# Performance work log

Hardware: AMD Instinct MI355X
Metric: run time of the kernel (lower is better)

Reference implementation:

```python
import jax, jax.numpy as jnp
import numpy as np

N_NODES = 50000
N_EDGES = 800000
NUM_GRAPHS = 512
IN_DIM = 128
HID = 128
OUT_DIM = 1


def setup_inputs() -> dict:
    key = jax.random.key(0)
    ks = jax.random.split(key, 8)
    x = jax.random.normal(ks[0], (N_NODES, IN_DIM), dtype=jnp.float32)
    edge_index = jax.random.randint(ks[1], (2, N_EDGES), 0, N_NODES, dtype=jnp.int64)
    batch = jnp.sort(jax.random.randint(ks[2], (N_NODES,), 0, NUM_GRAPHS, dtype=jnp.int64))
    s1 = 1.0 / np.sqrt(IN_DIM)
    s2 = 1.0 / np.sqrt(HID)
    W1 = jax.random.normal(ks[3], (IN_DIM, HID), dtype=jnp.float32) * s1
    b1 = jnp.zeros((HID,), dtype=jnp.float32)
    W2 = jax.random.normal(ks[4], (HID, HID), dtype=jnp.float32) * s2
    b2 = jnp.zeros((HID,), dtype=jnp.float32)
    Wl = jax.random.normal(ks[5], (HID, OUT_DIM), dtype=jnp.float32) * s2
    bl = jnp.zeros((OUT_DIM,), dtype=jnp.float32)
    return {"x": x, "edge_index": edge_index, "batch": batch,
            "W1": W1, "b1": b1, "W2": W2, "b2": b2, "Wl": Wl, "bl": bl}


def _gcn_conv(x, src, dst, norm, W, b):
    # GCNConv: D^{-1/2}(A+I)D^{-1/2} X W + b (self-loops already in src/dst)
    h = x @ W                                    # [N, H]
    msg = h[src] * norm[:, None]                 # gather + edge-normalize
    agg = jax.ops.segment_sum(msg, dst, num_segments=N_NODES)  # scatter-add
    return agg + b


def reference(x, edge_index, batch, W1, b1, W2, b2, Wl, bl):
    loops = jnp.arange(N_NODES, dtype=edge_index.dtype)
    src = jnp.concatenate([edge_index[0], loops])
    dst = jnp.concatenate([edge_index[1], loops])
    deg = jax.ops.segment_sum(jnp.ones_like(dst, dtype=x.dtype), dst, num_segments=N_NODES)
    dinv = jax.lax.rsqrt(deg)                    # deg >= 1 due to self-loops
    norm = dinv[src] * dinv[dst]                 # symmetric normalization per edge

    h = jax.nn.relu(_gcn_conv(x, src, dst, norm, W1, b1))
    h = jax.nn.relu(_gcn_conv(h, src, dst, norm, W2, b2))

    # global_mean_pool over graph ids
    sums = jax.ops.segment_sum(h, batch, num_segments=NUM_GRAPHS)
    cnts = jax.ops.segment_sum(jnp.ones((N_NODES,), dtype=h.dtype), batch, num_segments=NUM_GRAPHS)
    pooled = sums / jnp.maximum(cnts, 1.0)[:, None]

    out = jax.nn.sigmoid(pooled @ Wl + bl)       # [G, 1]
    return out.squeeze(1)                        # [G]
```

## Files before the change

### kernel.cpp

```cpp
#include <hip/hip_runtime.h>
#include <hip/hip_bf16.h>

#define N_NODES 50000
#define N_EDGES 800000
#define NUM_GRAPHS 512
#define MAXDEG 64
#define EPB 4096
#define P1_BLOCKS 196
#define NBUCK 256
#define NPB 196

typedef short short8 __attribute__((ext_vector_type(8)));
typedef unsigned short u16x8 __attribute__((ext_vector_type(8)));
typedef float f32x4 __attribute__((ext_vector_type(4)));

__device__ __forceinline__ unsigned short f2bu(float f) {
    __hip_bfloat16 h = __float2bfloat16(f);
    return *reinterpret_cast<unsigned short*>(&h);
}
__device__ __forceinline__ float bu2f(unsigned short u) {
    unsigned int v = ((unsigned int)u) << 16;
    float f;
    __builtin_memcpy(&f, &v, 4);
    return f;
}

__global__ __launch_bounds__(256) void bin_k(const int* __restrict__ ei,
                                             unsigned int* __restrict__ staging,
                                             int* __restrict__ cnts_tbl,
                                             int* __restrict__ offs_tbl,
                                             unsigned short* __restrict__ hs1,
                                             unsigned short* __restrict__ hs2) {
    __shared__ unsigned int st[EPB];
    __shared__ int cnt[NBUCK], cur[NBUCK], scan[NBUCK];
    int b = blockIdx.x, t = threadIdx.x;
    if (b == 0 && t < 64)
        ((unsigned int*)(hs1 + (size_t)N_NODES * 128))[t] = 0u;
    if (b == 1 && t < 64)
        ((unsigned int*)(hs2 + (size_t)N_NODES * 128))[t] = 0u;
    cnt[t] = 0;
    __syncthreads();

    int e0 = b * EPB;
    int srcv[16], dstv[16], bk[16];
#pragma unroll
    for (int k = 0; k < 16; ++k) {
        int e = e0 + k * 256 + t;
        bool ok = e < N_EDGES;
        srcv[k] = ok ? ei[e] : 0;
        dstv[k] = ok ? ei[N_EDGES + e] : 0;
        bk[k] = ok ? (dstv[k] / NPB) : -1;
        if (ok) atomicAdd(&cnt[bk[k]], 1);
    }
    __syncthreads();
    scan[t] = cnt[t];
    __syncthreads();
    for (int off = 1; off < 256; off <<= 1) {
        int u = t >= off ? scan[t - off] : 0;
        __syncthreads();
        scan[t] += u;
        __syncthreads();
    }
    int excl = scan[t] - cnt[t];
    cur[t] = excl;
    cnts_tbl[t * P1_BLOCKS + b] = cnt[t];
    offs_tbl[t * P1_BLOCKS + b] = excl;
    __syncthreads();
#pragma unroll
    for (int k = 0; k < 16; ++k) {
        if (bk[k] >= 0) {
            int pos = atomicAdd(&cur[bk[k]], 1);
            int dl = dstv[k] - bk[k] * NPB;
            st[pos] = (unsigned int)srcv[k] | ((unsigned int)dl << 16);
        }
    }
    __syncthreads();
    unsigned int* gout = staging + (size_t)b * EPB;
    for (int i = t; i < EPB; i += 256) gout[i] = st[i];
}

__global__ __launch_bounds__(256) void adjbuild_k(const unsigned int* __restrict__ staging,
                                                  const int* __restrict__ cnts_tbl,
                                                  const int* __restrict__ offs_tbl,
                                                  unsigned short* __restrict__ adj,
                                                  int* __restrict__ cnt,
                                                  float* __restrict__ dinv,
                                                  const float* __restrict__ W1,
                                                  const float* __restrict__ W2,
                                                  unsigned short* __restrict__ W1t,
                                                  unsigned short* __restrict__ W2t) {
    int b = blockIdx.x, t = threadIdx.x;
    if (b >= NBUCK) {
        int wb = b - NBUCK;
        const float* W = wb < 64 ? W1 : W2;
        unsigned short* Wt = wb < 64 ? W1t : W2t;
        int idx = (wb & 63) * 256 + t;
        int k = idx >> 7, n = idx & 127;
        Wt[n * 128 + k] = f2bu(W[idx]);
        return;
    }
    __shared__ unsigned short adjL[NPB * MAXDEG];
    __shared__ int cntL[NPB];
    __shared__ int segStart[P1_BLOCKS + 1];
    __shared__ int segOff[P1_BLOCKS];
    __shared__ int tmp[256];

    if (t < NPB) cntL[t] = 0;
    int c = t < P1_BLOCKS ? cnts_tbl[b * P1_BLOCKS + t] : 0;
    if (t < P1_BLOCKS) segOff[t] = offs_tbl[b * P1_BLOCKS + t];
    tmp[t] = c;
    __syncthreads();
    for (int off = 1; off < 256; off <<= 1) {
        int u = t >= off ? tmp[t - off] : 0;
        __syncthreads();
        tmp[t] += u;
        __syncthreads();
    }
    if (t < P1_BLOCKS) segStart[t] = tmp[t] - c;
    if (t == 0) segStart[P1_BLOCKS] = tmp[P1_BLOCKS - 1];
    __syncthreads();

    int T = segStart[P1_BLOCKS];
    for (int f = t; f < T; f += 256) {
        int lo = 0, hi = P1_BLOCKS;
        while (hi - lo > 1) {
            int m = (lo + hi) >> 1;
            if (segStart[m] <= f) lo = m; else hi = m;
        }
        unsigned int p = staging[(size_t)lo * EPB + segOff[lo] + (f - segStart[lo])];
        int src = p & 0xFFFF;
        int dl = p >> 16;
        int slot = atomicAdd(&cntL[dl], 1);
        if (slot < MAXDEG - 1) adjL[dl * MAXDEG + slot] = (unsigned short)src;
    }
    __syncthreads();

    int nodeBase = b * NPB;
    if (t < NPB) {
        int node = nodeBase + t;
        int cc = cntL[t];
        int ec = cc < MAXDEG - 1 ? cc : MAXDEG - 1;
        adjL[t * MAXDEG + ec] = (unsigned short)node;
        int tot = ec + 1, tot4 = (tot + 3) & ~3;
        for (int s = tot; s < tot4; ++s) adjL[t * MAXDEG + s] = (unsigned short)N_NODES;
        if (node < N_NODES) {
            cnt[node] = cc;
            dinv[node] = rsqrtf((float)cc + 1.0f);
        }
    }
    __syncthreads();
    unsigned int* g = (unsigned int*)(adj + (size_t)nodeBase * MAXDEG);
    const unsigned int* l = (const unsigned int*)adjL;
    for (int i = t; i < NPB * MAXDEG / 2; i += 256) g[i] = l[i];
}

__global__ __launch_bounds__(256) void gemm_k(const float* __restrict__ Ap,
                                              const unsigned short* __restrict__ Wt,
                                              const float* __restrict__ dinv,
                                              unsigned short* __restrict__ C) {
    __shared__ unsigned short Wl[128 * 136];
    int t = threadIdx.x;
    for (int idx = t; idx < 2048; idx += 256) {
        int n = idx >> 4, c = idx & 15;
        *(u16x8*)(Wl + n * 136 + c * 8) = *(const u16x8*)(Wt + n * 128 + c * 8);
    }
    __syncthreads();

    int wave = t >> 6, lane = t & 63, quad = lane >> 4, ln = lane & 15;
    int rb = blockIdx.x * 128 + wave * 16;

    short8 a[2][4];
#pragma unroll
    for (int mt = 0; mt < 2; ++mt) {
        int r = rb + mt * 64 + ln;
        r = r < N_NODES ? r : N_NODES - 1;
        const float* arow = Ap + (size_t)r * 128 + quad * 8;
#pragma unroll
        for (int ks = 0; ks < 4; ++ks) {
            float4 v0 = *(const float4*)(arow + ks * 32);
            float4 v1 = *(const float4*)(arow + ks * 32 + 4);
            short8 av;
            av[0] = (short)f2bu(v0.x); av[1] = (short)f2bu(v0.y);
            av[2] = (short)f2bu(v0.z); av[3] = (short)f2bu(v0.w);
            av[4] = (short)f2bu(v1.x); av[5] = (short)f2bu(v1.y);
            av[6] = (short)f2bu(v1.z); av[7] = (short)f2bu(v1.w);
            a[mt][ks] = av;
        }
    }

    f32x4 acc[2][8];
#pragma unroll
    for (int mt = 0; mt < 2; ++mt)
#pragma unroll
        for (int ct = 0; ct < 8; ++ct) acc[mt][ct] = (f32x4){0.f, 0.f, 0.f, 0.f};

#pragma unroll
    for (int ks = 0; ks < 4; ++ks)
#pragma unroll
        for (int ct = 0; ct < 8; ++ct) {
            short8 b = *(const short8*)(Wl + (ct * 16 + ln) * 136 + ks * 32 + quad * 8);
            acc[0][ct] = __builtin_amdgcn_mfma_f32_16x16x32_bf16(a[0][ks], b, acc[0][ct], 0, 0, 0);
            acc[1][ct] = __builtin_amdgcn_mfma_f32_16x16x32_bf16(a[1][ks], b, acc[1][ct], 0, 0, 0);
        }

#pragma unroll
    for (int mt = 0; mt < 2; ++mt) {
#pragma unroll
        for (int rr = 0; rr < 4; ++rr) {
            int r = rb + mt * 64 + quad * 4 + rr;
            if (r >= N_NODES) continue;
            float dv = dinv[r];
#pragma unroll
            for (int ct = 0; ct < 8; ++ct)
                C[(size_t)r * 128 + ct * 16 + ln] = f2bu(acc[mt][ct][rr] * dv);
        }
    }
}

__global__ __launch_bounds__(256) void agg_gemm_k(const unsigned short* __restrict__ hs1,
                                                  const unsigned short* __restrict__ adj,
                                                  const int* __restrict__ cnt,
                                                  const float* __restrict__ dinv,
                                                  const float* __restrict__ bias,
                                                  const unsigned short* __restrict__ W2t,
                                                  unsigned short* __restrict__ hs2) {
    __shared__ unsigned short h1t[16 * 136];
    int t = threadIdx.x, wave = t >> 6, lane = t & 63;
    int quad = lane >> 4, fl = lane & 15;
    int nb = blockIdx.x * 16;

    float4 b0 = *(const float4*)(bias + fl * 8);
    float4 b1f = *(const float4*)(bias + fl * 8 + 4);

#pragma unroll
    for (int q = 0; q < 4; ++q) {
        int lr = wave * 4 + q;
        int node = nb + lr;
        int idxv = (int)adj[node * MAXDEG + lane];
        int c = cnt[node];
        int ec = c < MAXDEG - 1 ? c : MAXDEG - 1;
        int iters = (ec + 4) >> 2;

        float acc[8];
#pragma unroll
        for (int j = 0; j < 8; ++j) acc[j] = 0.f;

        int i = 0;
        for (; i + 4 <= iters; i += 4) {
            int s0 = __shfl(idxv, i * 4 + quad, 64);
            int s1 = __shfl(idxv, i * 4 + 4 + quad, 64);
            int s2 = __shfl(idxv, i * 4 + 8 + quad, 64);
            int s3 = __shfl(idxv, i * 4 + 12 + quad, 64);
            u16x8 v0 = *(const u16x8*)(hs1 + (size_t)s0 * 128 + fl * 8);
            u16x8 v1 = *(const u16x8*)(hs1 + (size_t)s1 * 128 + fl * 8);
            u16x8 v2 = *(const u16x8*)(hs1 + (size_t)s2 * 128 + fl * 8);
            u16x8 v3 = *(const u16x8*)(hs1 + (size_t)s3 * 128 + fl * 8);
#pragma unroll
            for (int j = 0; j < 8; ++j)
                acc[j] += (bu2f(v0[j]) + bu2f(v1[j])) + (bu2f(v2[j]) + bu2f(v3[j]));
        }
        for (; i < iters; ++i) {
            int s0 = __shfl(idxv, i * 4 + quad, 64);
            u16x8 v0 = *(const u16x8*)(hs1 + (size_t)s0 * 128 + fl * 8);
#pragma unroll
            for (int j = 0; j < 8; ++j) acc[j] += bu2f(v0[j]);
        }
#pragma unroll
        for (int j = 0; j < 8; ++j) {
            acc[j] += __shfl_xor(acc[j], 16, 64);
            acc[j] += __shfl_xor(acc[j], 32, 64);
        }
        if (quad == 0) {
            float dv = dinv[node];
            u16x8 o;
            o[0] = f2bu(fmaxf(acc[0] * dv + b0.x, 0.f));
            o[1] = f2bu(fmaxf(acc[1] * dv + b0.y, 0.f));
            o[2] = f2bu(fmaxf(acc[2] * dv + b0.z, 0.f));
            o[3] = f2bu(fmaxf(acc[3] * dv + b0.w, 0.f));
            o[4] = f2bu(fmaxf(acc[4] * dv + b1f.x, 0.f));
            o[5] = f2bu(fmaxf(acc[5] * dv + b1f.y, 0.f));
            o[6] = f2bu(fmaxf(acc[6] * dv + b1f.z, 0.f));
            o[7] = f2bu(fmaxf(acc[7] * dv + b1f.w, 0.f));
            *(u16x8*)(h1t + lr * 136 + fl * 8) = o;
        }
    }
    __syncthreads();

    int ln = fl;
    short8 a[4];
#pragma unroll
    for (int ks = 0; ks < 4; ++ks)
        a[ks] = *(const short8*)(h1t + ln * 136 + ks * 32 + quad * 8);

    f32x4 acc2[2];
    acc2[0] = (f32x4){0.f, 0.f, 0.f, 0.f};
    acc2[1] = (f32x4){0.f, 0.f, 0.f, 0.f};
#pragma unroll
    for (int ks = 0; ks < 4; ++ks)
#pragma unroll
        for (int ct = 0; ct < 2; ++ct) {
            short8 b = *(const short8*)(W2t + (wave * 32 + ct * 16 + ln) * 128 + ks * 32 + quad * 8);
            acc2[ct] = __builtin_amdgcn_mfma_f32_16x16x32_bf16(a[ks], b, acc2[ct], 0, 0, 0);
        }

    float dvr[4];
#pragma unroll
    for (int rr = 0; rr < 4; ++rr) dvr[rr] = dinv[nb + quad * 4 + rr];
#pragma unroll
    for (int ct = 0; ct < 2; ++ct)
#pragma unroll
        for (int rr = 0; rr < 4; ++rr) {
            int node = nb + quad * 4 + rr;
            hs2[(size_t)node * 128 + wave * 32 + ct * 16 + ln] = f2bu(acc2[ct][rr] * dvr[rr]);
        }
}

__global__ __launch_bounds__(256) void agg_dot_k(const unsigned short* __restrict__ hs,
                                                 const unsigned short* __restrict__ adj,
                                                 const int* __restrict__ cnt,
                                                 const float* __restrict__ dinv,
                                                 const float* __restrict__ bias,
                                                 const float* __restrict__ Wl,
                                                 float* __restrict__ pnode) {
    int wave = threadIdx.x >> 6, lane = threadIdx.x & 63;
    int node = blockIdx.x * 4 + wave;
    int quad = lane >> 4, fl = lane & 15;
    int idx = (int)adj[node * MAXDEG + lane];
    int c = cnt[node];
    int ec = c < MAXDEG - 1 ? c : MAXDEG - 1;
    int iters = (ec + 4) >> 2;

    float acc[8];
#pragma unroll
    for (int j = 0; j < 8; ++j) acc[j] = 0.f;

    int i = 0;
    for (; i + 4 <= iters; i += 4) {
        int s0 = __shfl(idx, i * 4 + quad, 64);
        int s1 = __shfl(idx, i * 4 + 4 + quad, 64);
        int s2 = __shfl(idx, i * 4 + 8 + quad, 64);
        int s3 = __shfl(idx, i * 4 + 12 + quad, 64);
        u16x8 v0 = *(const u16x8*)(hs + (size_t)s0 * 128 + fl * 8);
        u16x8 v1 = *(const u16x8*)(hs + (size_t)s1 * 128 + fl * 8);
        u16x8 v2 = *(const u16x8*)(hs + (size_t)s2 * 128 + fl * 8);
        u16x8 v3 = *(const u16x8*)(hs + (size_t)s3 * 128 + fl * 8);
#pragma unroll
        for (int j = 0; j < 8; ++j)
            acc[j] += (bu2f(v0[j]) + bu2f(v1[j])) + (bu2f(v2[j]) + bu2f(v3[j]));
    }
    for (; i < iters; ++i) {
        int s0 = __shfl(idx, i * 4 + quad, 64);
        u16x8 v0 = *(const u16x8*)(hs + (size_t)s0 * 128 + fl * 8);
#pragma unroll
        for (int j = 0; j < 8; ++j) acc[j] += bu2f(v0[j]);
    }

#pragma unroll
    for (int j = 0; j < 8; ++j) {
        acc[j] += __shfl_xor(acc[j], 16, 64);
        acc[j] += __shfl_xor(acc[j], 32, 64);
    }

    if (quad == 0) {
        float dv = dinv[node];
        float4 b0 = *(const float4*)(bias + fl * 8);
        float4 b1 = *(const float4*)(bias + fl * 8 + 4);
        float4 w0 = *(const float4*)(Wl + fl * 8);
        float4 w1 = *(const float4*)(Wl + fl * 8 + 4);
        float p = fmaxf(acc[0] * dv + b0.x, 0.f) * w0.x
                + fmaxf(acc[1] * dv + b0.y, 0.f) * w0.y
                + fmaxf(acc[2] * dv + b0.z, 0.f) * w0.z
                + fmaxf(acc[3] * dv + b0.w, 0.f) * w0.w
                + fmaxf(acc[4] * dv + b1.x, 0.f) * w1.x
                + fmaxf(acc[5] * dv + b1.y, 0.f) * w1.y
                + fmaxf(acc[6] * dv + b1.z, 0.f) * w1.z
                + fmaxf(acc[7] * dv + b1.w, 0.f) * w1.w;
        p += __shfl_xor(p, 1, 64);
        p += __shfl_xor(p, 2, 64);
        p += __shfl_xor(p, 4, 64);
        p += __shfl_xor(p, 8, 64);
        if (fl == 0) pnode[node] = p;
    }
}

__device__ __forceinline__ int lb(const int* a, int n, int v) {
    int lo = 0, hi = n;
    while (lo < hi) {
        int m = (lo + hi) >> 1;
        if (a[m] < v) lo = m + 1;
        else hi = m;
    }
    return lo;
}

__global__ __launch_bounds__(64) void final_k(const float* __restrict__ pnode,
                                              const int* __restrict__ batch,
                                              const float* __restrict__ bl,
                                              float* __restrict__ out) {
    int g = blockIdx.x, t = threadIdx.x;
    int lo = lb(batch, N_NODES, g), hi = lb(batch, N_NODES, g + 1);
    float s = 0.f;
    for (int r = lo + t; r < hi; r += 64) s += pnode[r];
#pragma unroll
    for (int o = 32; o > 0; o >>= 1) s += __shfl_down(s, o, 64);
    if (t == 0) {
        float cf = (float)(hi - lo);
        float z = s / fmaxf(cf, 1.f) + bl[0];
        out[g] = 1.f / (1.f + expf(-z));
    }
}

extern "C" void kernel_launch(void* const* d_in, const int* in_sizes, int n_in,
                              void* d_out, int out_size, void* d_ws, size_t ws_size,
                              hipStream_t stream) {
    const float* x = (const float*)d_in[0];
    const int* ei = (const int*)d_in[1];
    const int* batch = (const int*)d_in[2];
    const float* W1 = (const float*)d_in[3];
    const float* b1 = (const float*)d_in[4];
    const float* W2 = (const float*)d_in[5];
    const float* b2 = (const float*)d_in[6];
    const float* Wl = (const float*)d_in[7];
    const float* bl = (const float*)d_in[8];
    float* out = (float*)d_out;

    char* ws = (char*)d_ws;
    unsigned int* staging = (unsigned int*)(ws + 0x0);
    int* cnts_tbl = (int*)(ws + 0x310000);
    int* offs_tbl = (int*)(ws + 0x341000);
    unsigned short* adj = (unsigned short*)(ws + 0x372000);
    int* cnt = (int*)(ws + 0x992000);
    float* dinv = (float*)(ws + 0x9C3000);
    unsigned short* W1t = (unsigned short*)(ws + 0x9F4000);
    unsigned short* W2t = (unsigned short*)(ws + 0x9FC000);
    float* pnode = (float*)(ws + 0xA04000);
    unsigned short* hs1 = (unsigned short*)(ws + 0xA36000);
    unsigned short* hs2 = (unsigned short*)(ws + 0x1672000);

    bin_k<<<P1_BLOCKS, 256, 0, stream>>>(ei, staging, cnts_tbl, offs_tbl, hs1, hs2);
    adjbuild_k<<<NBUCK + 128, 256, 0, stream>>>(staging, cnts_tbl, offs_tbl,
                                                adj, cnt, dinv, W1, W2, W1t, W2t);

    gemm_k<<<(N_NODES + 127) / 128, 256, 0, stream>>>(x, W1t, dinv, hs1);
    agg_gemm_k<<<N_NODES / 16, 256, 0, stream>>>(hs1, adj, cnt, dinv, b1, W2t, hs2);
    agg_dot_k<<<N_NODES / 4, 256, 0, stream>>>(hs2, adj, cnt, dinv, b2, Wl, pnode);

    final_k<<<NUM_GRAPHS, 64, 0, stream>>>(pnode, batch, bl, out);
}
```

Measured before the change: 194.5 us.

## Split fused layer-2 aggregate+GEMM into separate aggregation and bf16 GEMM kernels

Replaces the fused agg_gemm kernel (16 nodes per block, aggregation then per-block MFMA with W2 read from global) with a one-node-per-wave aggregation kernel that writes h1 to global. A templated gemm_k that accepts bf16 input then applies W2 with W staged in LDS. This drops the block-wide barrier and the repeated W2 global reads per small block, and lets each phase use its own grid shape. The cost is an extra kernel launch and a round trip of the 50000x128 bf16 intermediate through memory.

Result: faster. 190.1 us (-2.3%).

```diff
diff --git a/kernel.cpp b/kernel.cpp
--- a/kernel.cpp
+++ b/kernel.cpp
@@ -154,7 +154,8 @@
     for (int i = t; i < NPB * MAXDEG / 2; i += 256) g[i] = l[i];
 }
 
-__global__ __launch_bounds__(256) void gemm_k(const float* __restrict__ Ap,
+template <bool F32A>
+__global__ __launch_bounds__(256) void gemm_k(const void* __restrict__ Ap,
                                               const unsigned short* __restrict__ Wt,
                                               const float* __restrict__ dinv,
                                               unsigned short* __restrict__ C) {
@@ -174,17 +175,23 @@
     for (int mt = 0; mt < 2; ++mt) {
         int r = rb + mt * 64 + ln;
         r = r < N_NODES ? r : N_NODES - 1;
-        const float* arow = Ap + (size_t)r * 128 + quad * 8;
-#pragma unroll
-        for (int ks = 0; ks < 4; ++ks) {
-            float4 v0 = *(const float4*)(arow + ks * 32);
-            float4 v1 = *(const float4*)(arow + ks * 32 + 4);
-            short8 av;
-            av[0] = (short)f2bu(v0.x); av[1] = (short)f2bu(v0.y);
-            av[2] = (short)f2bu(v0.z); av[3] = (short)f2bu(v0.w);
-            av[4] = (short)f2bu(v1.x); av[5] = (short)f2bu(v1.y);
-            av[6] = (short)f2bu(v1.z); av[7] = (short)f2bu(v1.w);
-            a[mt][ks] = av;
+        if (F32A) {
+            const float* arow = (const float*)Ap + (size_t)r * 128 + quad * 8;
+#pragma unroll
+            for (int ks = 0; ks < 4; ++ks) {
+                float4 v0 = *(const float4*)(arow + ks * 32);
+                float4 v1 = *(const float4*)(arow + ks * 32 + 4);
+                short8 av;
+                av[0] = (short)f2bu(v0.x); av[1] = (short)f2bu(v0.y);
+                av[2] = (short)f2bu(v0.z); av[3] = (short)f2bu(v0.w);
+                av[4] = (short)f2bu(v1.x); av[5] = (short)f2bu(v1.y);
+                av[6] = (short)f2bu(v1.z); av[7] = (short)f2bu(v1.w);
+                a[mt][ks] = av;
+            }
+        } else {
+            const unsigned short* arow = (const unsigned short*)Ap + (size_t)r * 128 + quad * 8;
+#pragma unroll
+            for (int ks = 0; ks < 4; ++ks) a[mt][ks] = *(const short8*)(arow + ks * 32);
         }
     }
 
@@ -217,102 +224,66 @@
     }
 }
 
-__global__ __launch_bounds__(256) void agg_gemm_k(const unsigned short* __restrict__ hs1,
-                                                  const unsigned short* __restrict__ adj,
-                                                  const int* __restrict__ cnt,
-                                                  const float* __restrict__ dinv,
-                                                  const float* __restrict__ bias,
-                                                  const unsigned short* __restrict__ W2t,
-                                                  unsigned short* __restrict__ hs2) {
-    __shared__ unsigned short h1t[16 * 136];
-    int t = threadIdx.x, wave = t >> 6, lane = t & 63;
+__global__ __launch_bounds__(256) void agg1_k(const unsigned short* __restrict__ hs,
+                                              const unsigned short* __restrict__ adj,
+                                              const int* __restrict__ cnt,
+                                              const float* __restrict__ dinv,
+                                              const float* __restrict__ bias,
+                                              unsigned short* __restrict__ out) {
+    int wave = threadIdx.x >> 6, lane = threadIdx.x & 63;
+    int node = blockIdx.x * 4 + wave;
     int quad = lane >> 4, fl = lane & 15;
-    int nb = blockIdx.x * 16;
-
-    float4 b0 = *(const float4*)(bias + fl * 8);
-    float4 b1f = *(const float4*)(bias + fl * 8 + 4);
-
-#pragma unroll
-    for (int q = 0; q < 4; ++q) {
-        int lr = wave * 4 + q;
-        int node = nb + lr;
-        int idxv = (int)adj[node * MAXDEG + lane];
-        int c = cnt[node];
-        int ec = c < MAXDEG - 1 ? c : MAXDEG - 1;
-        int iters = (ec + 4) >> 2;
-
-        float acc[8];
-#pragma unroll
-        for (int j = 0; j < 8; ++j) acc[j] = 0.f;
-
-        int i = 0;
-        for (; i + 4 <= iters; i += 4) {
-            int s0 = __shfl(idxv, i * 4 + quad, 64);
-            int s1 = __shfl(idxv, i * 4 + 4 + quad, 64);
-            int s2 = __shfl(idxv, i * 4 + 8 + quad, 64);
-            int s3 = __shfl(idxv, i * 4 + 12 + quad, 64);
-            u16x8 v0 = *(const u16x8*)(hs1 + (size_t)s0 * 128 + fl * 8);
-            u16x8 v1 = *(const u16x8*)(hs1 + (size_t)s1 * 128 + fl * 8);
-            u16x8 v2 = *(const u16x8*)(hs1 + (size_t)s2 * 128 + fl * 8);
-            u16x8 v3 = *(const u16x8*)(hs1 + (size_t)s3 * 128 + fl * 8);
-#pragma unroll
-            for (int j = 0; j < 8; ++j)
-                acc[j] += (bu2f(v0[j]) + bu2f(v1[j])) + (bu2f(v2[j]) + bu2f(v3[j]));
-        }
-        for (; i < iters; ++i) {
-            int s0 = __shfl(idxv, i * 4 + quad, 64);
-            u16x8 v0 = *(const u16x8*)(hs1 + (size_t)s0 * 128 + fl * 8);
-#pragma unroll
-            for (int j = 0; j < 8; ++j) acc[j] += bu2f(v0[j]);
-        }
-#pragma unroll
-        for (int j = 0; j < 8; ++j) {
-            acc[j] += __shfl_xor(acc[j], 16, 64);
-            acc[j] += __shfl_xor(acc[j], 32, 64);
-        }
-        if (quad == 0) {
-            float dv = dinv[node];
-            u16x8 o;
-            o[0] = f2bu(fmaxf(acc[0] * dv + b0.x, 0.f));
-            o[1] = f2bu(fmaxf(acc[1] * dv + b0.y, 0.f));
-            o[2] = f2bu(fmaxf(acc[2] * dv + b0.z, 0.f));
-            o[3] = f2bu(fmaxf(acc[3] * dv + b0.w, 0.f));
-            o[4] = f2bu(fmaxf(acc[4] * dv + b1f.x, 0.f));
-            o[5] = f2bu(fmaxf(acc[5] * dv + b1f.y, 0.f));
-            o[6] = f2bu(fmaxf(acc[6] * dv + b1f.z, 0.f));
-            o[7] = f2bu(fmaxf(acc[7] * dv + b1f.w, 0.f));
-            *(u16x8*)(h1t + lr * 136 + fl * 8) = o;
-        }
-    }
-    __syncthreads();
-
-    int ln = fl;
-    short8 a[4];
-#pragma unroll
-    for (int ks = 0; ks < 4; ++ks)
-        a[ks] = *(const short8*)(h1t + ln * 136 + ks * 32 + quad * 8);
-
-    f32x4 acc2[2];
-    acc2[0] = (f32x4){0.f, 0.f, 0.f, 0.f};
-    acc2[1] = (f32x4){0.f, 0.f, 0.f, 0.f};
-#pragma unroll
-    for (int ks = 0; ks < 4; ++ks)
-#pragma unroll
-        for (int ct = 0; ct < 2; ++ct) {
-            short8 b = *(const short8*)(W2t + (wave * 32 + ct * 16 + ln) * 128 + ks * 32 + quad * 8);
-            acc2[ct] = __builtin_amdgcn_mfma_f32_16x16x32_bf16(a[ks], b, acc2[ct], 0, 0, 0);
-        }
-
-    float dvr[4];
-#pragma unroll
-    for (int rr = 0; rr < 4; ++rr) dvr[rr] = dinv[nb + quad * 4 + rr];
-#pragma unroll
-    for (int ct = 0; ct < 2; ++ct)
-#pragma unroll
-        for (int rr = 0; rr < 4; ++rr) {
-            int node = nb + quad * 4 + rr;
-            hs2[(size_t)node * 128 + wave * 32 + ct * 16 + ln] = f2bu(acc2[ct][rr] * dvr[rr]);
-        }
+    int idx = (int)adj[node * MAXDEG + lane];
+    int c = cnt[node];
+    int ec = c < MAXDEG - 1 ? c : MAXDEG - 1;
+    int iters = (ec + 4) >> 2;
+
+    float acc[8];
+#pragma unroll
+    for (int j = 0; j < 8; ++j) acc[j] = 0.f;
+
+    int i = 0;
+    for (; i + 4 <= iters; i += 4) {
+        int s0 = __shfl(idx, i * 4 + quad, 64);
+        int s1 = __shfl(idx, i * 4 + 4 + quad, 64);
+        int s2 = __shfl(idx, i * 4 + 8 + quad, 64);
+        int s3 = __shfl(idx, i * 4 + 12 + quad, 64);
+        u16x8 v0 = *(const u16x8*)(hs + (size_t)s0 * 128 + fl * 8);
+        u16x8 v1 = *(const u16x8*)(hs + (size_t)s1 * 128 + fl * 8);
+        u16x8 v2 = *(const u16x8*)(hs + (size_t)s2 * 128 + fl * 8);
+        u16x8 v3 = *(const u16x8*)(hs + (size_t)s3 * 128 + fl * 8);
+#pragma unroll
+        for (int j = 0; j < 8; ++j)
+            acc[j] += (bu2f(v0[j]) + bu2f(v1[j])) + (bu2f(v2[j]) + bu2f(v3[j]));
+    }
+    for (; i < iters; ++i) {
+        int s0 = __shfl(idx, i * 4 + quad, 64);
+        u16x8 v0 = *(const u16x8*)(hs + (size_t)s0 * 128 + fl * 8);
+#pragma unroll
+        for (int j = 0; j < 8; ++j) acc[j] += bu2f(v0[j]);
+    }
+
+#pragma unroll
+    for (int j = 0; j < 8; ++j) {
+        acc[j] += __shfl_xor(acc[j], 16, 64);
+        acc[j] += __shfl_xor(acc[j], 32, 64);
+    }
+
+    if (quad == 0) {
+        float dv = dinv[node];
+        float4 b0 = *(const float4*)(bias + fl * 8);
+        float4 b1 = *(const float4*)(bias + fl * 8 + 4);
+        u16x8 o;
+        o[0] = f2bu(fmaxf(acc[0] * dv + b0.x, 0.f));
+        o[1] = f2bu(fmaxf(acc[1] * dv + b0.y, 0.f));
+        o[2] = f2bu(fmaxf(acc[2] * dv + b0.z, 0.f));
+        o[3] = f2bu(fmaxf(acc[3] * dv + b0.w, 0.f));
+        o[4] = f2bu(fmaxf(acc[4] * dv + b1.x, 0.f));
+        o[5] = f2bu(fmaxf(acc[5] * dv + b1.y, 0.f));
+        o[6] = f2bu(fmaxf(acc[6] * dv + b1.z, 0.f));
+        o[7] = f2bu(fmaxf(acc[7] * dv + b1.w, 0.f));
+        *(u16x8*)(out + (size_t)node * 128 + fl * 8) = o;
+    }
 }
 
 __global__ __launch_bounds__(256) void agg_dot_k(const unsigned short* __restrict__ hs,
@@ -435,14 +406,16 @@
     unsigned short* W2t = (unsigned short*)(ws + 0x9FC000);
     float* pnode = (float*)(ws + 0xA04000);
     unsigned short* hs1 = (unsigned short*)(ws + 0xA36000);
-    unsigned short* hs2 = (unsigned short*)(ws + 0x1672000);
+    unsigned short* h1 = (unsigned short*)(ws + 0x1672000);
+    unsigned short* hs2 = (unsigned short*)(ws + 0x22AE000);
 
     bin_k<<<P1_BLOCKS, 256, 0, stream>>>(ei, staging, cnts_tbl, offs_tbl, hs1, hs2);
     adjbuild_k<<<NBUCK + 128, 256, 0, stream>>>(staging, cnts_tbl, offs_tbl,
                                                 adj, cnt, dinv, W1, W2, W1t, W2t);
 
-    gemm_k<<<(N_NODES + 127) / 128, 256, 0, stream>>>(x, W1t, dinv, hs1);
-    agg_gemm_k<<<N_NODES / 16, 256, 0, stream>>>(hs1, adj, cnt, dinv, b1, W2t, hs2);
+    gemm_k<true><<<(N_NODES + 127) / 128, 256, 0, stream>>>(x, W1t, dinv, hs1);
+    agg1_k<<<N_NODES / 4, 256, 0, stream>>>(hs1, adj, cnt, dinv, b1, h1);
+    gemm_k<false><<<(N_NODES + 127) / 128, 256, 0, stream>>>(h1, W2t, dinv, hs2);
     agg_dot_k<<<N_NODES / 4, 256, 0, stream>>>(hs2, adj, cnt, dinv, b2, Wl, pnode);
 
     final_k<<<NUM_GRAPHS, 64, 0, stream>>>(pnode, batch, bl, out);
```
